# Kernel optimization log

Measured on AMD Instinct MI355X. Metric: run time of the kernel, lower is better.

Reference implementation:

```python
import jax, jax.numpy as jnp
import numpy as np

B, S, E, H = 2, 2048, 1024, 16
D = E // H  # head size


def setup_inputs() -> dict:
    key = jax.random.key(0)
    ks = jax.random.split(key, 11)
    s = 1.0 / np.sqrt(E)
    inp = {
        "q": jax.random.normal(ks[0], (B, S, E), jnp.float32),
        "k": jax.random.normal(ks[1], (B, S, E), jnp.float32),
        "v": jax.random.normal(ks[2], (B, S, E), jnp.float32),
        # nn.Linear weights stored [out, in] like torch
        "Wq": jax.random.uniform(ks[3], (E, E), jnp.float32, -s, s),
        "bq": jax.random.uniform(ks[4], (E,), jnp.float32, -s, s),
        "Wk": jax.random.uniform(ks[5], (E, E), jnp.float32, -s, s),
        "bk": jax.random.uniform(ks[6], (E,), jnp.float32, -s, s),
        "Wv": jax.random.uniform(ks[7], (E, E), jnp.float32, -s, s),
        "bv": jax.random.uniform(ks[8], (E,), jnp.float32, -s, s),
        "Wl": jax.random.uniform(ks[9], (E, E), jnp.float32, -s, s),
        "bl": jax.random.uniform(ks[10], (E,), jnp.float32, -s, s),
    }
    return inp


def _split_heads(x):  # [B,S,E] -> [B,H,S,D]
    b, s, _ = x.shape
    return x.reshape(b, s, H, D).transpose(0, 2, 1, 3)


def reference(q, k, v, Wq, bq, Wk, bk, Wv, bv, Wl, bl):
    scale = E ** (-0.5)  # NOTE: embedding_dim scale, faithful to source
    Q = _split_heads(q @ Wq.T + bq)  # [B,H,S,D]
    K = _split_heads(k @ Wk.T + bk)
    V = _split_heads(v @ Wv.T + bv)
    a = jnp.einsum("bhqd,bhkd->bhqk", Q, K) * scale
    a = jax.nn.softmax(a, axis=-1)
    # masked=True: causal-mask AFTER softmax, then renormalize rows
    mask = jnp.tril(jnp.ones((S, S), dtype=bool))
    a = jnp.where(mask, a, 0.0)
    a = a / jnp.sum(a, axis=-1, keepdims=True)
    o = jnp.einsum("bhqk,bhkd->bhqd", a, V)  # [B,H,S,D]
    o = o.transpose(0, 2, 1, 3).reshape(B, S, E)
    return o @ Wl.T + bl  # dropout = identity in eval
```

## Files before the change

### kernel.cpp

```cpp
#include <hip/hip_runtime.h>
#include <hip/hip_bf16.h>

#define Bx 2
#define Sx 2048
#define Ex 1024
#define Hx 16
#define Dx 64

typedef __attribute__((ext_vector_type(8))) short s16x8;
typedef __attribute__((ext_vector_type(4))) short s16x4;
typedef __attribute__((ext_vector_type(4))) float f32x4;

__device__ __forceinline__ short f2bf(float f) {
    union { float f; unsigned u; } x; x.f = f;
    unsigned r = (x.u + 0x7fffu + ((x.u >> 16) & 1u)) >> 16;
    return (short)(r & 0xffffu);
}

__device__ __forceinline__ s16x8 pack8(const float* p) {
    s16x8 r;
#pragma unroll
    for (int i = 0; i < 8; ++i) r[i] = f2bf(p[i]);
    return r;
}

__device__ __forceinline__ void gload16(const void* g, void* l) {
    __builtin_amdgcn_global_load_lds(
        (const __attribute__((address_space(1))) unsigned int*)g,
        (__attribute__((address_space(3))) unsigned int*)l, 16, 0, 0);
}

__global__ __launch_bounds__(256) void cvt_kernel(
    const float* __restrict__ q, const float* __restrict__ k, const float* __restrict__ v,
    const float* __restrict__ wq, const float* __restrict__ wk, const float* __restrict__ wv,
    const float* __restrict__ wl, short* __restrict__ dst)
{
    int b = blockIdx.x;
    const float* src; size_t doff; int cb;
    if (b < 6144) {
        int wch = b >> 11;
        src = wch == 0 ? q : (wch == 1 ? k : v);
        cb = b & 2047; doff = (size_t)wch * 4194304;
    } else {
        int wch = (b - 6144) >> 9;
        src = wch == 0 ? wq : (wch == 1 ? wk : (wch == 2 ? wv : wl));
        cb = (b - 6144) & 511; doff = 12582912 + (size_t)wch * 1048576;
    }
    size_t base = (size_t)cb * 2048 + threadIdx.x * 8;
    float tmp[8];
    *(f32x4*)&tmp[0] = *(const f32x4*)&src[base];
    *(f32x4*)&tmp[4] = *(const f32x4*)&src[base + 4];
    *(s16x8*)&dst[doff + base] = pack8(tmp);
}

__global__ __launch_bounds__(256) void qkv_fast(
    const short* __restrict__ xq, const short* __restrict__ xk, const short* __restrict__ xv,
    const short* __restrict__ wq, const short* __restrict__ wk, const short* __restrict__ wv,
    const float* __restrict__ bq, const float* __restrict__ bk, const float* __restrict__ bv,
    short* __restrict__ Qo, short* __restrict__ Ko, short* __restrict__ Vto)
{
    __shared__ short Al[2][128 * 32];
    __shared__ short Wl[2][128 * 32];
    const int bx = blockIdx.x;
    const int proj = bx >> 3;
    const int n0 = (bx & 7) * 128, m0 = blockIdx.y * 128;
    const short* A = proj == 0 ? xq : (proj == 1 ? xk : xv);
    const short* W = proj == 0 ? wq : (proj == 1 ? wk : wv);
    const float* bias = proj == 0 ? bq : (proj == 1 ? bk : bv);
    const int t = threadIdx.x, lane = t & 63, wid = t >> 6;
    const int wm = (wid >> 1) * 64, wn = (wid & 1) * 64;
    f32x4 acc[4][4] = {};
    const int srow = lane >> 2;
    const int csrc = ((lane & 3) ^ (srow & 3)) << 3;

#define QSTAGE(buf, k0_) do {                                                           \
        int rr0_ = (wid * 2 + 0) * 16 + srow;                                           \
        int rr1_ = (wid * 2 + 1) * 16 + srow;                                           \
        gload16(&A[(size_t)(m0 + rr0_) * 1024 + (k0_) + csrc], &Al[buf][(wid * 2 + 0) * 512]); \
        gload16(&W[(size_t)(n0 + rr0_) * 1024 + (k0_) + csrc], &Wl[buf][(wid * 2 + 0) * 512]); \
        gload16(&A[(size_t)(m0 + rr1_) * 1024 + (k0_) + csrc], &Al[buf][(wid * 2 + 1) * 512]); \
        gload16(&W[(size_t)(n0 + rr1_) * 1024 + (k0_) + csrc], &Wl[buf][(wid * 2 + 1) * 512]); \
    } while (0)

    int cur = 0;
    QSTAGE(0, 0);
#pragma unroll 1
    for (int it = 0; it < 32; ++it) {
        if (it < 31) {
            QSTAGE(cur ^ 1, (it + 1) * 32);
            asm volatile("s_waitcnt vmcnt(4)" ::: "memory");
        } else {
            asm volatile("s_waitcnt vmcnt(0)" ::: "memory");
        }
        __builtin_amdgcn_s_barrier();
        __builtin_amdgcn_sched_barrier(0);
        s16x8 af[4], bf[4];
#pragma unroll
        for (int i = 0; i < 4; ++i) {
            int ra = wm + i * 16 + (lane & 15);
            int rb = wn + i * 16 + (lane & 15);
            af[i] = *(const s16x8*)&Al[cur][ra * 32 + (((lane >> 4) ^ (ra & 3)) << 3)];
            bf[i] = *(const s16x8*)&Wl[cur][rb * 32 + (((lane >> 4) ^ (rb & 3)) << 3)];
        }
#pragma unroll
        for (int mi = 0; mi < 4; ++mi)
#pragma unroll
            for (int ni = 0; ni < 4; ++ni)
                acc[mi][ni] = __builtin_amdgcn_mfma_f32_16x16x32_bf16(af[mi], bf[ni], acc[mi][ni], 0, 0, 0);
        __builtin_amdgcn_s_barrier();
        cur ^= 1;
    }
#undef QSTAGE

    const int lg = lane >> 4, l15 = lane & 15;
    const float sc = (proj == 0) ? 0.045084220027780106f : 1.0f;
    if (proj < 2) {
        short* out = proj == 0 ? Qo : Ko;
#pragma unroll
        for (int ni = 0; ni < 4; ++ni) {
            int n = n0 + wn + ni * 16 + l15;
            float bvv = bias[n];
            int h = n >> 6, d = n & 63;
#pragma unroll
            for (int mi = 0; mi < 4; ++mi)
#pragma unroll
                for (int i = 0; i < 4; ++i) {
                    int m = m0 + wm + mi * 16 + (lg << 2) + i;
                    int b = m >> 11, s = m & 2047;
                    out[(((size_t)(b * Hx + h)) * Sx + s) * Dx + d] = f2bf((acc[mi][ni][i] + bvv) * sc);
                }
        }
    } else {
#pragma unroll
        for (int ni = 0; ni < 4; ++ni) {
            int n = n0 + wn + ni * 16 + l15;
            float bvv = bias[n];
            int h = n >> 6, d = n & 63;
#pragma unroll
            for (int mi = 0; mi < 4; ++mi) {
                int m = m0 + wm + mi * 16 + (lg << 2);
                int b = m >> 11, s0 = m & 2047;
                s16x4 pk;
#pragma unroll
                for (int i = 0; i < 4; ++i) pk[i] = f2bf(acc[mi][ni][i] + bvv);
                *(s16x4*)&Vto[(((size_t)(b * Hx + h)) * Dx + d) * Sx + s0] = pk;
            }
        }
    }
}

__global__ __launch_bounds__(256) void final_fast(
    const short* __restrict__ Ab, const short* __restrict__ Wb,
    const float* __restrict__ bias, float* __restrict__ out)
{
    __shared__ short Al[2][128 * 32];
    __shared__ short Wl[2][64 * 32];
    const int n0 = blockIdx.x * 64, m0 = blockIdx.y * 128;
    const int t = threadIdx.x, lane = t & 63, wid = t >> 6;
    const int wm = wid * 32;
    f32x4 acc[2][4] = {};
    const int srow = lane >> 2;
    const int csrc = ((lane & 3) ^ (srow & 3)) << 3;

#define FSTAGE(buf, k0_) do {                                                           \
        int rr0_ = (wid * 2 + 0) * 16 + srow;                                           \
        int rr1_ = (wid * 2 + 1) * 16 + srow;                                           \
        int rw_ = wid * 16 + srow;                                                      \
        gload16(&Ab[(size_t)(m0 + rr0_) * 1024 + (k0_) + csrc], &Al[buf][(wid * 2 + 0) * 512]); \
        gload16(&Ab[(size_t)(m0 + rr1_) * 1024 + (k0_) + csrc], &Al[buf][(wid * 2 + 1) * 512]); \
        gload16(&Wb[(size_t)(n0 + rw_) * 1024 + (k0_) + csrc],  &Wl[buf][wid * 512]);   \
    } while (0)

    int cur = 0;
    FSTAGE(0, 0);
#pragma unroll 1
    for (int it = 0; it < 32; ++it) {
        if (it < 31) {
            FSTAGE(cur ^ 1, (it + 1) * 32);
            asm volatile("s_waitcnt vmcnt(3)" ::: "memory");
        } else {
            asm volatile("s_waitcnt vmcnt(0)" ::: "memory");
        }
        __builtin_amdgcn_s_barrier();
        __builtin_amdgcn_sched_barrier(0);
        s16x8 af[2], bf[4];
#pragma unroll
        for (int mi = 0; mi < 2; ++mi) {
            int ra = wm + mi * 16 + (lane & 15);
            af[mi] = *(const s16x8*)&Al[cur][ra * 32 + (((lane >> 4) ^ (ra & 3)) << 3)];
        }
#pragma unroll
        for (int ni = 0; ni < 4; ++ni) {
            int rb = ni * 16 + (lane & 15);
            bf[ni] = *(const s16x8*)&Wl[cur][rb * 32 + (((lane >> 4) ^ (rb & 3)) << 3)];
        }
#pragma unroll
        for (int mi = 0; mi < 2; ++mi)
#pragma unroll
            for (int ni = 0; ni < 4; ++ni)
                acc[mi][ni] = __builtin_amdgcn_mfma_f32_16x16x32_bf16(af[mi], bf[ni], acc[mi][ni], 0, 0, 0);
        __builtin_amdgcn_s_barrier();
        cur ^= 1;
    }
#undef FSTAGE
#pragma unroll
    for (int ni = 0; ni < 4; ++ni) {
        int n = n0 + ni * 16 + (lane & 15);
        float bvv = bias[n];
#pragma unroll
        for (int mi = 0; mi < 2; ++mi)
#pragma unroll
            for (int i = 0; i < 4; ++i) {
                int m = m0 + wm + mi * 16 + ((lane >> 4) << 2) + i;
                out[(size_t)m * 1024 + n] = acc[mi][ni][i] + bvv;
            }
    }
}

__global__ __launch_bounds__(256) void attn_kernel(
    const short* __restrict__ Q, const short* __restrict__ K,
    const short* __restrict__ Vt, short* __restrict__ O)
{
    __shared__ short Kl[2][64 * 64];
    __shared__ short Vl[2][64 * 64];
    __shared__ short Pl[4][16][72];
    const int bx = blockIdx.x;
    const int bh = blockIdx.y, b = bh >> 4, h = bh & 15;
    const short* Qh = Q + (size_t)bh * Sx * Dx;
    const short* Kh = K + (size_t)bh * Sx * Dx;
    const short* Vh = Vt + (size_t)bh * Dx * Sx;
    const int t = threadIdx.x, lane = t & 63, wid = t >> 6;
    const int l15 = lane & 15, lg = lane >> 4;
    const int r8 = lane >> 3;
    const int csrc = ((lane & 7) ^ r8) << 3;
    const int rr0 = wid * 16 + r8;

#define STAGE(buf, tk_) do {                                                          \
        int kb_ = (tk_) * 64;                                                         \
        gload16(&Kh[(size_t)(kb_ + rr0) * Dx + csrc],     &Kl[buf][(wid * 2 + 0) * 512]); \
        gload16(&Kh[(size_t)(kb_ + rr0 + 8) * Dx + csrc], &Kl[buf][(wid * 2 + 1) * 512]); \
        gload16(&Vh[(size_t)rr0 * Sx + kb_ + csrc],       &Vl[buf][(wid * 2 + 0) * 512]); \
        gload16(&Vh[(size_t)(rr0 + 8) * Sx + kb_ + csrc], &Vl[buf][(wid * 2 + 1) * 512]); \
    } while (0)

#pragma unroll 1
    for (int phase = 0; phase < 2; ++phase) {
        const int qblk = phase ? (31 - bx) : bx;
        const int nkv = qblk + 1;
        const int qbase = qblk * 64 + wid * 16;

        s16x8 qf[2];
#pragma unroll
        for (int ks = 0; ks < 2; ++ks)
            qf[ks] = *(const s16x8*)&Qh[(size_t)(qbase + l15) * Dx + ks * 32 + (lg << 3)];

        f32x4 of[4] = {};
        float lrun[4] = {0.f, 0.f, 0.f, 0.f};

        int cur = 0;
        STAGE(0, 0);

#pragma unroll 1
        for (int tk = 0; tk < nkv; ++tk) {
            const int kb = tk * 64;
            if (tk + 1 < nkv) {
                STAGE(cur ^ 1, tk + 1);
                asm volatile("s_waitcnt vmcnt(4)" ::: "memory");
            } else {
                asm volatile("s_waitcnt vmcnt(0)" ::: "memory");
            }
            __builtin_amdgcn_s_barrier();
            __builtin_amdgcn_sched_barrier(0);

            f32x4 sf[4];
#pragma unroll
            for (int ni = 0; ni < 4; ++ni) {
                int r = ni * 16 + l15;
                s16x8 b0 = *(const s16x8*)&Kl[cur][r * 64 + ((lg ^ (r & 7)) << 3)];
                s16x8 b1 = *(const s16x8*)&Kl[cur][r * 64 + (((4 + lg) ^ (r & 7)) << 3)];
                f32x4 z = {};
                z = __builtin_amdgcn_mfma_f32_16x16x32_bf16(qf[0], b0, z, 0, 0, 0);
                sf[ni] = __builtin_amdgcn_mfma_f32_16x16x32_bf16(qf[1], b1, z, 0, 0, 0);
            }
            if (tk == nkv - 1) {
#pragma unroll
                for (int ni = 0; ni < 4; ++ni)
#pragma unroll
                    for (int i = 0; i < 4; ++i) {
                        int qrow = qbase + (lg << 2) + i;
                        int kcol = kb + ni * 16 + l15;
                        sf[ni][i] = (kcol <= qrow) ? sf[ni][i] : -1e30f;
                    }
            }
#pragma unroll
            for (int ni = 0; ni < 4; ++ni)
#pragma unroll
                for (int i = 0; i < 4; ++i)
                    sf[ni][i] = __builtin_exp2f(sf[ni][i]);
#pragma unroll
            for (int i = 0; i < 4; ++i) {
                float rs = (sf[0][i] + sf[1][i]) + (sf[2][i] + sf[3][i]);
#pragma unroll
                for (int off = 1; off < 16; off <<= 1) rs += __shfl_xor(rs, off, 64);
                lrun[i] += rs;
            }
#pragma unroll
            for (int ni = 0; ni < 4; ++ni)
#pragma unroll
                for (int i = 0; i < 4; ++i)
                    Pl[wid][(lg << 2) + i][ni * 16 + l15] = f2bf(sf[ni][i]);
            __builtin_amdgcn_sched_barrier(0);
            s16x8 pa[2];
#pragma unroll
            for (int ks = 0; ks < 2; ++ks)
                pa[ks] = *(const s16x8*)&Pl[wid][l15][ks * 32 + (lg << 3)];
#pragma unroll
            for (int ni = 0; ni < 4; ++ni) {
                int r = ni * 16 + l15;
                s16x8 v0 = *(const s16x8*)&Vl[cur][r * 64 + ((lg ^ (r & 7)) << 3)];
                s16x8 v1 = *(const s16x8*)&Vl[cur][r * 64 + (((4 + lg) ^ (r & 7)) << 3)];
                of[ni] = __builtin_amdgcn_mfma_f32_16x16x32_bf16(pa[0], v0, of[ni], 0, 0, 0);
                of[ni] = __builtin_amdgcn_mfma_f32_16x16x32_bf16(pa[1], v1, of[ni], 0, 0, 0);
            }
            __builtin_amdgcn_s_barrier();
            cur ^= 1;
        }

#pragma unroll
        for (int ni = 0; ni < 4; ++ni)
#pragma unroll
            for (int i = 0; i < 4; ++i) {
                int row = qbase + (lg << 2) + i;
                int d = ni * 16 + l15;
                O[((size_t)(b * Sx + row)) * Ex + h * Dx + d] = f2bf(of[ni][i] / lrun[i]);
            }
    }
#undef STAGE
}

extern "C" void kernel_launch(void* const* d_in, const int* in_sizes, int n_in,
                              void* d_out, int out_size, void* d_ws, size_t ws_size,
                              hipStream_t stream) {
    const float* q  = (const float*)d_in[0];
    const float* k  = (const float*)d_in[1];
    const float* v  = (const float*)d_in[2];
    const float* Wq = (const float*)d_in[3];
    const float* bq = (const float*)d_in[4];
    const float* Wk = (const float*)d_in[5];
    const float* bk = (const float*)d_in[6];
    const float* Wv = (const float*)d_in[7];
    const float* bv = (const float*)d_in[8];
    const float* Wl = (const float*)d_in[9];
    const float* bl = (const float*)d_in[10];

    short* ws = (short*)d_ws;
    short* xq  = ws;
    short* xk  = ws + 4194304;
    short* xv  = ws + 8388608;
    short* wqb = ws + 12582912;
    short* wkb = ws + 13631488;
    short* wvb = ws + 14680064;
    short* wlb = ws + 15728640;
    short* Qb  = ws + 16777216;
    short* Kb  = ws + 20971520;
    short* Vtb = ws + 25165824;
    short* Ob  = ws + 29360128;

    cvt_kernel<<<8192, 256, 0, stream>>>(q, k, v, Wq, Wk, Wv, Wl, ws);
    qkv_fast<<<dim3(24, 32), dim3(256), 0, stream>>>(xq, xk, xv, wqb, wkb, wvb,
                                                     bq, bk, bv, Qb, Kb, Vtb);
    attn_kernel<<<dim3(16, 32), dim3(256), 0, stream>>>(Qb, Kb, Vtb, Ob);
    final_fast<<<dim3(16, 32), dim3(256), 0, stream>>>(Ob, wlb, bl, (float*)d_out);
}
```

Before: 249.6 us.

## Remap blocks across XCDs, raise MFMA wave priority, defer softmax row-sum reduction

```diff
diff --git a/kernel.cpp b/kernel.cpp
--- a/kernel.cpp
+++ b/kernel.cpp
@@ -61,9 +61,11 @@
 {
     __shared__ short Al[2][128 * 32];
     __shared__ short Wl[2][128 * 32];
-    const int bx = blockIdx.x;
-    const int proj = bx >> 3;
-    const int n0 = (bx & 7) * 128, m0 = blockIdx.y * 128;
+    const int lin = blockIdx.x + blockIdx.y * 24;
+    const int xcd = lin & 7, idx = lin >> 3;
+    const int bxs = xcd * 3 + idx % 3;
+    const int proj = bxs >> 3;
+    const int n0 = (bxs & 7) * 128, m0 = (idx / 3) * 128;
     const short* A = proj == 0 ? xq : (proj == 1 ? xk : xv);
     const short* W = proj == 0 ? wq : (proj == 1 ? wk : wv);
     const float* bias = proj == 0 ? bq : (proj == 1 ? bk : bv);
@@ -102,11 +104,13 @@
             af[i] = *(const s16x8*)&Al[cur][ra * 32 + (((lane >> 4) ^ (ra & 3)) << 3)];
             bf[i] = *(const s16x8*)&Wl[cur][rb * 32 + (((lane >> 4) ^ (rb & 3)) << 3)];
         }
+        __builtin_amdgcn_s_setprio(1);
 #pragma unroll
         for (int mi = 0; mi < 4; ++mi)
 #pragma unroll
             for (int ni = 0; ni < 4; ++ni)
                 acc[mi][ni] = __builtin_amdgcn_mfma_f32_16x16x32_bf16(af[mi], bf[ni], acc[mi][ni], 0, 0, 0);
+        __builtin_amdgcn_s_setprio(0);
         __builtin_amdgcn_s_barrier();
         cur ^= 1;
     }
@@ -155,7 +159,10 @@
 {
     __shared__ short Al[2][128 * 32];
     __shared__ short Wl[2][64 * 32];
-    const int n0 = blockIdx.x * 64, m0 = blockIdx.y * 128;
+    const int lin = blockIdx.x + (blockIdx.y << 4);
+    const int xcd = lin & 7, idx = lin >> 3;
+    const int n0 = ((xcd << 1) + (idx & 1)) * 64;
+    const int m0 = (idx >> 1) * 128;
     const int t = threadIdx.x, lane = t & 63, wid = t >> 6;
     const int wm = wid * 32;
     f32x4 acc[2][4] = {};
@@ -194,11 +201,13 @@
             int rb = ni * 16 + (lane & 15);
             bf[ni] = *(const s16x8*)&Wl[cur][rb * 32 + (((lane >> 4) ^ (rb & 3)) << 3)];
         }
+        __builtin_amdgcn_s_setprio(1);
 #pragma unroll
         for (int mi = 0; mi < 2; ++mi)
 #pragma unroll
             for (int ni = 0; ni < 4; ++ni)
                 acc[mi][ni] = __builtin_amdgcn_mfma_f32_16x16x32_bf16(af[mi], bf[ni], acc[mi][ni], 0, 0, 0);
+        __builtin_amdgcn_s_setprio(0);
         __builtin_amdgcn_s_barrier();
         cur ^= 1;
     }
@@ -224,8 +233,11 @@
     __shared__ short Kl[2][64 * 64];
     __shared__ short Vl[2][64 * 64];
     __shared__ short Pl[4][16][72];
-    const int bx = blockIdx.x;
-    const int bh = blockIdx.y, b = bh >> 4, h = bh & 15;
+    const int lin = blockIdx.x + (blockIdx.y << 4);
+    const int xcd = lin & 7, idx = lin >> 3;
+    const int bh = (xcd << 2) + (idx & 3);
+    const int bx = idx >> 2;
+    const int b = bh >> 4, h = bh & 15;
     const short* Qh = Q + (size_t)bh * Sx * Dx;
     const short* Kh = K + (size_t)bh * Sx * Dx;
     const short* Vh = Vt + (size_t)bh * Dx * Sx;
@@ -255,7 +267,7 @@
             qf[ks] = *(const s16x8*)&Qh[(size_t)(qbase + l15) * Dx + ks * 32 + (lg << 3)];
 
         f32x4 of[4] = {};
-        float lrun[4] = {0.f, 0.f, 0.f, 0.f};
+        float psum[4] = {0.f, 0.f, 0.f, 0.f};
 
         int cur = 0;
         STAGE(0, 0);
@@ -273,6 +285,7 @@
             __builtin_amdgcn_sched_barrier(0);
 
             f32x4 sf[4];
+            __builtin_amdgcn_s_setprio(1);
 #pragma unroll
             for (int ni = 0; ni < 4; ++ni) {
                 int r = ni * 16 + l15;
@@ -282,6 +295,7 @@
                 z = __builtin_amdgcn_mfma_f32_16x16x32_bf16(qf[0], b0, z, 0, 0, 0);
                 sf[ni] = __builtin_amdgcn_mfma_f32_16x16x32_bf16(qf[1], b1, z, 0, 0, 0);
             }
+            __builtin_amdgcn_s_setprio(0);
             if (tk == nkv - 1) {
 #pragma unroll
                 for (int ni = 0; ni < 4; ++ni)
@@ -298,12 +312,8 @@
                 for (int i = 0; i < 4; ++i)
                     sf[ni][i] = __builtin_exp2f(sf[ni][i]);
 #pragma unroll
-            for (int i = 0; i < 4; ++i) {
-                float rs = (sf[0][i] + sf[1][i]) + (sf[2][i] + sf[3][i]);
-#pragma unroll
-                for (int off = 1; off < 16; off <<= 1) rs += __shfl_xor(rs, off, 64);
-                lrun[i] += rs;
-            }
+            for (int i = 0; i < 4; ++i)
+                psum[i] += (sf[0][i] + sf[1][i]) + (sf[2][i] + sf[3][i]);
 #pragma unroll
             for (int ni = 0; ni < 4; ++ni)
 #pragma unroll
@@ -314,6 +324,7 @@
 #pragma unroll
             for (int ks = 0; ks < 2; ++ks)
                 pa[ks] = *(const s16x8*)&Pl[wid][l15][ks * 32 + (lg << 3)];
+            __builtin_amdgcn_s_setprio(1);
 #pragma unroll
             for (int ni = 0; ni < 4; ++ni) {
                 int r = ni * 16 + l15;
@@ -322,10 +333,19 @@
                 of[ni] = __builtin_amdgcn_mfma_f32_16x16x32_bf16(pa[0], v0, of[ni], 0, 0, 0);
                 of[ni] = __builtin_amdgcn_mfma_f32_16x16x32_bf16(pa[1], v1, of[ni], 0, 0, 0);
             }
+            __builtin_amdgcn_s_setprio(0);
             __builtin_amdgcn_s_barrier();
             cur ^= 1;
         }
 
+        float lrun[4];
+#pragma unroll
+        for (int i = 0; i < 4; ++i) {
+            float rs = psum[i];
+#pragma unroll
+            for (int off = 1; off < 16; off <<= 1) rs += __shfl_xor(rs, off, 64);
+            lrun[i] = rs;
+        }
 #pragma unroll
         for (int ni = 0; ni < 4; ++ni)
 #pragma unroll
```

Measured after the change: 236.1 us. -5.4%, faster.
